# Performance work log

Hardware: AMD Instinct MI355X
Metric: run time of the kernel (lower is better)

Reference implementation:

```python
import jax, jax.numpy as jnp
import numpy as np

B, S, D, V = 32, 1024, 768, 32000


def setup_inputs() -> dict:
    key = jax.random.key(0)
    ks = jax.random.split(key, 12)
    scale = 0.02
    return {
        "tokens": jax.random.randint(ks[0], (B, S), 0, V, dtype=jnp.int32),
        "mask": jax.random.randint(ks[1], (B, S), 0, 2, dtype=jnp.int32),
        "emb": jax.random.normal(ks[2], (V, D), dtype=jnp.float32) * scale,
        "wq": jax.random.normal(ks[3], (D, D), dtype=jnp.float32) * scale,
        "wk": jax.random.normal(ks[4], (D, D), dtype=jnp.float32) * scale,
        "wv": jax.random.normal(ks[5], (D, D), dtype=jnp.float32) * scale,
        "ln_g": jnp.ones((D,), dtype=jnp.float32),
        "ln_b": jnp.zeros((D,), dtype=jnp.float32),
        "w1": jax.random.normal(ks[6], (D, D), dtype=jnp.float32) * scale,
        "b1": jnp.zeros((D,), dtype=jnp.float32),
        "wh": jax.random.normal(ks[7], (D, 2), dtype=jnp.float32) * scale,
        "bh": jnp.zeros((2,), dtype=jnp.float32),
    }


def reference(tokens, mask, emb, wq, wk, wv, ln_g, ln_b, w1, b1, wh, bh):
    # embedding lookup: [B,S,D]
    x = emb[tokens]
    q = x @ wq
    k = x @ wk
    v = x @ wv
    # unscaled attention scores: [B,S,S]
    s = jnp.einsum("bsd,btd->bst", q, k)
    # additive padding mask (mask==1 -> -1e9), broadcast over query dim
    s = s + (-1e9) * mask.astype(s.dtype)[:, None, :]
    a = jax.nn.softmax(s, axis=-1)
    o = jnp.einsum("bst,btd->bsd", a, v)
    # classify on first token
    cls = o[:, 0, :]  # [B,D]
    mu = jnp.mean(cls, axis=-1, keepdims=True)
    var = jnp.var(cls, axis=-1, keepdims=True)
    h = (cls - mu) * jax.lax.rsqrt(var + 1e-5) * ln_g + ln_b
    h = jax.nn.gelu(h @ w1 + b1, approximate=False)
    logits = h @ wh + bh  # [B,2]
    return (logits, a)
```

## Files before the change

kernel.cpp:

```cpp
#include <hip/hip_runtime.h>
#include <hip/hip_bf16.h>

#define NB 32
#define SS 1024
#define DD 768

typedef __attribute__((ext_vector_type(8))) short bf16x8;
typedef __attribute__((ext_vector_type(4))) float f32x4;

__device__ inline ushort f2bf(float f) {
    union { float f; unsigned u; } x;
    x.f = f;
    unsigned r = (x.u + 0x7fffu + ((x.u >> 16) & 1u)) >> 16;
    return (ushort)r;
}

#define GLOBAL_PTR(x) ((const __attribute__((address_space(1))) void*)(x))
#define LDS_PTR(x)    ((__attribute__((address_space(3))) void*)(x))

__global__ void k_cvt(const float* __restrict__ wq, const float* __restrict__ wk,
                      ushort* __restrict__ wqb, ushort* __restrict__ wkb) {
    const int i = (blockIdx.x * 256 + threadIdx.x) * 4;
    const float* src = blockIdx.y ? wk : wq;
    ushort* dst = blockIdx.y ? wkb : wqb;
    const float4 v = *(const float4*)(src + i);
    ushort4 o;
    o.x = f2bf(v.x); o.y = f2bf(v.y); o.z = f2bf(v.z); o.w = f2bf(v.w);
    *(ushort4*)(dst + i) = o;
}

__global__ void k_gather(const int* __restrict__ tokens, const float* __restrict__ emb,
                         ushort* __restrict__ xb) {
    int i = (blockIdx.x * 256 + threadIdx.x) * 4;
    int row = i / DD;
    int col = i - row * DD;
    int tok = tokens[row];
    const float4 v = *(const float4*)(emb + (size_t)tok * DD + col);
    ushort4 o;
    o.x = f2bf(v.x); o.y = f2bf(v.y); o.z = f2bf(v.z); o.w = f2bf(v.w);
    *(ushort4*)(xb + (size_t)row * DD + col) = o;
}

__global__ __launch_bounds__(256, 2) void k_gemm_s(const ushort* __restrict__ A,
                                                   const ushort* __restrict__ Bt,
                                                   ushort* __restrict__ Cb) {
    constexpr int BK = 64;
    __shared__ ushort As[2][128 * BK];
    __shared__ ushort Bs[2][128 * BK];
    const int tid = threadIdx.x;
    const int wave = tid >> 6, lane = tid & 63;
    const int bx = blockIdx.x, by = blockIdx.y;
    const size_t abase = (size_t)bx * 128 * DD;
    const size_t bbase = (size_t)by * 128 * DD;
    const int r = tid >> 3;
    const int cc = (tid & 7) * 8;

    auto stage = [&](int buf, int k0) {
#pragma unroll
        for (int i = 0; i < 4; i++) {
            __builtin_amdgcn_global_load_lds(GLOBAL_PTR(A + abase + (size_t)(r + i * 32) * DD + k0 + cc),
                                             LDS_PTR(&As[buf][(r + i * 32) * BK + cc]), 16, 0, 0);
            __builtin_amdgcn_global_load_lds(GLOBAL_PTR(Bt + bbase + (size_t)(r + i * 32) * DD + k0 + cc),
                                             LDS_PTR(&Bs[buf][(r + i * 32) * BK + cc]), 16, 0, 0);
        }
    };

    f32x4 acc[4][4] = {};
    const int wm = (wave >> 1) * 64, wn = (wave & 1) * 64;
    const int lr = lane & 15, lc = (lane >> 4) * 8;

    stage(0, 0);
    __syncthreads();
    int cur = 0;
#pragma unroll 1
    for (int k0 = 0; k0 < DD; k0 += BK) {
        if (k0 + BK < DD) stage(cur ^ 1, k0 + BK);
        const ushort* as = As[cur];
        const ushort* bs = Bs[cur];
#pragma unroll
        for (int kk = 0; kk < 2; kk++) {
            bf16x8 af[4], bfv[4];
#pragma unroll
            for (int m = 0; m < 4; m++)
                af[m] = *(const bf16x8*)(as + (wm + m * 16 + lr) * BK + kk * 32 + lc);
#pragma unroll
            for (int n = 0; n < 4; n++)
                bfv[n] = *(const bf16x8*)(bs + (wn + n * 16 + lr) * BK + kk * 32 + lc);
#pragma unroll
            for (int m = 0; m < 4; m++)
#pragma unroll
                for (int n = 0; n < 4; n++)
                    acc[m][n] = __builtin_amdgcn_mfma_f32_16x16x32_bf16(af[m], bfv[n], acc[m][n], 0, 0, 0);
        }
        __syncthreads();
        cur ^= 1;
    }
    const int rowbase = bx * 128 + wm + (lane >> 4) * 4;
    const int colbase = by * 128 + wn + (lane & 15);
#pragma unroll
    for (int m = 0; m < 4; m++)
#pragma unroll
        for (int n = 0; n < 4; n++)
#pragma unroll
            for (int j = 0; j < 4; j++)
                Cb[(size_t)(rowbase + m * 16 + j) * DD + colbase + n * 16] = f2bf(acc[m][n][j]);
}

#define HALF_USH (128 * 64)
__global__ __launch_bounds__(512, 2) void k_gemm256(const ushort* __restrict__ A,
                                                    const ushort* __restrict__ Bt,
                                                    ushort* __restrict__ Cb) {
    __shared__ ushort As[2][2][HALF_USH];
    __shared__ ushort Bs[2][2][HALF_USH];
    const int tid = threadIdx.x;
    const int wid = tid >> 6, lane = tid & 63;
    const int wm = wid >> 2, wn = wid & 3;
    const int la = lane & 15;

    const int bx = blockIdx.x, by = blockIdx.y;
    const ushort* Ag = A + (size_t)bx * 256 * DD;
    const ushort* Bg = Bt + (size_t)by * 256 * DD;

    int s_r[2], s_c[2], s_d[2];
#pragma unroll
    for (int l = 0; l < 2; l++) {
        const int L = (l * 512 + tid) * 16;
        const int r = L >> 7;
        const int cb = L & 127;
        s_r[l] = r;
        s_c[l] = (cb ^ ((r & 7) << 4)) >> 1;
        s_d[l] = L >> 1;
    }

    auto stage_half = [&](ushort* dst, const ushort* gsrc) {
#pragma unroll
        for (int l = 0; l < 2; l++)
            __builtin_amdgcn_global_load_lds(GLOBAL_PTR(gsrc + (size_t)s_r[l] * DD + s_c[l]),
                                             LDS_PTR(dst + s_d[l]), 16, 0, 0);
    };

    const int swz = (la & 7) << 4;
    const int off_k0 = (((lane >> 4) << 4) ^ swz) >> 1;
    const int off_k1 = ((64 | ((lane >> 4) << 4)) ^ swz) >> 1;

    f32x4 acc[8][4] = {};

    stage_half(&As[0][0][0], Ag);
    stage_half(&As[0][1][0], Ag + (size_t)128 * DD);
    stage_half(&Bs[0][0][0], Bg);
    stage_half(&Bs[0][1][0], Bg + (size_t)128 * DD);
    __syncthreads();

#pragma unroll 1
    for (int t = 0; t < 12; t++) {
        const int buf = t & 1;
        const ushort* Ah = &As[buf][wm][0];
        const ushort* Bh = &Bs[buf][wn >> 1][0];
        const int brow0 = (wn & 1) * 64;
        const int kt = (t + 1) * 64;
        bf16x8 bfv[4][2];
#pragma unroll
        for (int q = 0; q < 4; q++) {
            if (q == 0) {
#pragma unroll
                for (int n = 0; n < 4; n++) {
                    const int rr = brow0 + n * 16 + la;
                    bfv[n][0] = *(const bf16x8*)(Bh + rr * 64 + off_k0);
                    bfv[n][1] = *(const bf16x8*)(Bh + rr * 64 + off_k1);
                }
            }
            bf16x8 af[2][2];
#pragma unroll
            for (int dm = 0; dm < 2; dm++) {
                const int rr = (q * 2 + dm) * 16 + la;
                af[dm][0] = *(const bf16x8*)(Ah + rr * 64 + off_k0);
                af[dm][1] = *(const bf16x8*)(Ah + rr * 64 + off_k1);
            }
            if (t < 11) {
                if (q == 0) stage_half(&As[buf ^ 1][0][0], Ag + kt);
                if (q == 1) stage_half(&As[buf ^ 1][1][0], Ag + (size_t)128 * DD + kt);
                if (q == 2) stage_half(&Bs[buf ^ 1][0][0], Bg + kt);
                if (q == 3) stage_half(&Bs[buf ^ 1][1][0], Bg + (size_t)128 * DD + kt);
            }
            __builtin_amdgcn_s_setprio(1);
#pragma unroll
            for (int dm = 0; dm < 2; dm++)
#pragma unroll
                for (int n = 0; n < 4; n++)
#pragma unroll
                    for (int kk = 0; kk < 2; kk++)
                        acc[q * 2 + dm][n] = __builtin_amdgcn_mfma_f32_16x16x32_bf16(
                            af[dm][kk], bfv[n][kk], acc[q * 2 + dm][n], 0, 0, 0);
            __builtin_amdgcn_s_setprio(0);
            if (q < 3) __builtin_amdgcn_s_barrier();
        }
        __syncthreads();
    }

    const int rowbase = bx * 256 + wm * 128 + (lane >> 4) * 4;
    const int colbase = by * 256 + wn * 64 + la;
#pragma unroll
    for (int m = 0; m < 8; m++)
#pragma unroll
        for (int n = 0; n < 4; n++)
#pragma unroll
            for (int j = 0; j < 4; j++)
                Cb[(size_t)(rowbase + m * 16 + j) * DD + colbase + n * 16] = f2bf(acc[m][n][j]);
}

__global__ __launch_bounds__(512) void k_attn(const ushort* __restrict__ Y,
                                              const ushort* __restrict__ X,
                                              const int* __restrict__ mask,
                                              float* __restrict__ Aout) {
    __shared__ ushort Ash[2][64 * 64];
    __shared__ int    Msk[SS];
    __shared__ float  RedM[8][64];
    __shared__ float  RedS[8][64];

    const int tid = threadIdx.x;
    const int wid = tid >> 6, lane = tid & 63;
    const int la = lane & 15, lg = lane >> 4;

    const int wgid = blockIdx.x;
    const int g = wgid >> 7, w = wgid & 127;
    const int b = g * 8 + (w & 7);
    const int bx = w >> 3;
    const ushort* Ag = Y + (size_t)b * SS * DD + (size_t)bx * 64 * DD;
    const ushort* Bg = X + (size_t)b * SS * DD;
    float* Ao = Aout + (size_t)b * SS * SS + (size_t)bx * 64 * SS;

    Msk[tid] = mask[b * SS + tid];
    Msk[tid + 512] = mask[b * SS + tid + 512];

    const int r0 = tid >> 3;
    const int cb0 = (tid & 7) << 4;
    const int sc = (cb0 ^ ((r0 & 7) << 4)) >> 1;
    const int dofs = tid * 8;

    const int swz = (la & 7) << 4;
    const int off_k0 = ((lg << 4) ^ swz) >> 1;
    const int off_k1 = ((64 | (lg << 4)) ^ swz) >> 1;

    f32x4 acc[4][8] = {};

    __builtin_amdgcn_global_load_lds(GLOBAL_PTR(Ag + (size_t)r0 * DD + sc),
                                     LDS_PTR(&Ash[0][0] + dofs), 16, 0, 0);
    __syncthreads();

#pragma unroll 1
    for (int t = 0; t < 12; t++) {
        const int k0 = t * 64;
        if (t < 11)
            __builtin_amdgcn_global_load_lds(GLOBAL_PTR(Ag + (size_t)r0 * DD + (k0 + 64) + sc),
                                             LDS_PTR(&Ash[(t + 1) & 1][0] + dofs), 16, 0, 0);
        const ushort* ash = &Ash[t & 1][0];
        bf16x8 af[4][2];
#pragma unroll
        for (int m = 0; m < 4; m++) {
            const int rr = m * 16 + la;
            af[m][0] = *(const bf16x8*)(ash + rr * 64 + off_k0);
            af[m][1] = *(const bf16x8*)(ash + rr * 64 + off_k1);
        }
#pragma unroll
        for (int n = 0; n < 8; n++) {
            const ushort* bp = Bg + (size_t)(wid * 128 + n * 16 + la) * DD + k0 + lg * 8;
            const bf16x8 bf0 = *(const bf16x8*)bp;
            const bf16x8 bf1 = *(const bf16x8*)(bp + 32);
            __builtin_amdgcn_s_setprio(1);
#pragma unroll
            for (int m = 0; m < 4; m++) {
                acc[m][n] = __builtin_amdgcn_mfma_f32_16x16x32_bf16(af[m][0], bf0, acc[m][n], 0, 0, 0);
                acc[m][n] = __builtin_amdgcn_mfma_f32_16x16x32_bf16(af[m][1], bf1, acc[m][n], 0, 0, 0);
            }
            __builtin_amdgcn_s_setprio(0);
        }
        __syncthreads();
    }

    float bias[8];
#pragma unroll
    for (int n = 0; n < 8; n++)
        bias[n] = Msk[wid * 128 + n * 16 + la] ? -1e9f : 0.0f;

    float mxl[4][4];
#pragma unroll
    for (int m = 0; m < 4; m++)
#pragma unroll
        for (int j = 0; j < 4; j++) {
            float v = -3.4e38f;
#pragma unroll
            for (int n = 0; n < 8; n++) v = fmaxf(v, acc[m][n][j] + bias[n]);
#pragma unroll
            for (int off = 1; off < 16; off <<= 1) v = fmaxf(v, __shfl_xor(v, off));
            mxl[m][j] = v;
        }
    if (la == 0) {
#pragma unroll
        for (int m = 0; m < 4; m++)
#pragma unroll
            for (int j = 0; j < 4; j++)
                RedM[wid][m * 16 + lg * 4 + j] = mxl[m][j];
    }
    __syncthreads();
#pragma unroll
    for (int m = 0; m < 4; m++)
#pragma unroll
        for (int j = 0; j < 4; j++) {
            const int r = m * 16 + lg * 4 + j;
            float v = RedM[0][r];
#pragma unroll
            for (int ww = 1; ww < 8; ww++) v = fmaxf(v, RedM[ww][r]);
            mxl[m][j] = v;
        }

    float sml[4][4];
#pragma unroll
    for (int m = 0; m < 4; m++)
#pragma unroll
        for (int j = 0; j < 4; j++) {
            float s = 0.f;
#pragma unroll
            for (int n = 0; n < 8; n++) {
                const float e = __expf(acc[m][n][j] + bias[n] - mxl[m][j]);
                acc[m][n][j] = e;
                s += e;
            }
#pragma unroll
            for (int off = 1; off < 16; off <<= 1) s += __shfl_xor(s, off);
            sml[m][j] = s;
        }
    if (la == 0) {
#pragma unroll
        for (int m = 0; m < 4; m++)
#pragma unroll
            for (int j = 0; j < 4; j++)
                RedS[wid][m * 16 + lg * 4 + j] = sml[m][j];
    }
    __syncthreads();
#pragma unroll
    for (int m = 0; m < 4; m++)
#pragma unroll
        for (int j = 0; j < 4; j++) {
            const int r = m * 16 + lg * 4 + j;
            float s = RedS[0][r];
#pragma unroll
            for (int ww = 1; ww < 8; ww++) s += RedS[ww][r];
            const float inv = 1.0f / s;
#pragma unroll
            for (int n = 0; n < 8; n++)
                Ao[(size_t)r * SS + wid * 128 + n * 16 + la] = acc[m][n][j] * inv;
        }
}

__global__ __launch_bounds__(256) void k_xbar(const float* __restrict__ a, const int* __restrict__ tokens,
                                              const float* __restrict__ emb, float* __restrict__ part) {
    const int b = blockIdx.x >> 3, c = blockIdx.x & 7;
    __shared__ float a0s[128];
    __shared__ int toks[128];
    const int tid = threadIdx.x;
    if (tid < 128) {
        a0s[tid] = a[(size_t)b * SS * SS + c * 128 + tid];
        toks[tid] = tokens[b * SS + c * 128 + tid];
    }
    __syncthreads();
    float acc0 = 0.f, acc1 = 0.f, acc2 = 0.f;
#pragma unroll 4
    for (int t = 0; t < 128; t++) {
        const float at = a0s[t];
        const float* er = emb + (size_t)toks[t] * DD;
        acc0 = fmaf(at, er[tid], acc0);
        acc1 = fmaf(at, er[tid + 256], acc1);
        acc2 = fmaf(at, er[tid + 512], acc2);
    }
    float* p = part + ((size_t)c * NB + b) * DD;
    p[tid] = acc0; p[tid + 256] = acc1; p[tid + 512] = acc2;
}

__global__ __launch_bounds__(128) void k_cls(const float* __restrict__ part, const float* __restrict__ wv,
                                             float* __restrict__ cls) {
    const int b = blockIdx.y, tid = threadIdx.x;
    const int c = blockIdx.x * 128 + tid;
    __shared__ float xb[DD];
#pragma unroll
    for (int j = 0; j < 6; j++) {
        const int k = tid + j * 128;
        float s = 0.f;
#pragma unroll
        for (int p = 0; p < 8; p++) s += part[((size_t)p * NB + b) * DD + k];
        xb[k] = s;
    }
    __syncthreads();
    float acc = 0.f;
#pragma unroll 8
    for (int k = 0; k < DD; k++) acc = fmaf(xb[k], wv[(size_t)k * DD + c], acc);
    cls[(size_t)b * DD + c] = acc;
}

__device__ inline float block_sum256(float v, float* red, int tid) {
#pragma unroll
    for (int off = 32; off; off >>= 1) v += __shfl_xor(v, off);
    __syncthreads();
    if ((tid & 63) == 0) red[tid >> 6] = v;
    __syncthreads();
    return red[0] + red[1] + red[2] + red[3];
}

__global__ __launch_bounds__(256) void k_ln(const float* __restrict__ cls, const float* __restrict__ ln_g,
                                            const float* __restrict__ ln_b, float* __restrict__ hs) {
    const int b = blockIdx.x, tid = threadIdx.x;
    __shared__ float red[4];
    float v[3];
#pragma unroll
    for (int j = 0; j < 3; j++) v[j] = cls[(size_t)b * DD + tid + j * 256];
    const float mu = block_sum256(v[0] + v[1] + v[2], red, tid) * (1.0f / DD);
    float dv = 0.f;
#pragma unroll
    for (int j = 0; j < 3; j++) { const float d = v[j] - mu; dv += d * d; }
    __syncthreads();
    const float var = block_sum256(dv, red, tid) * (1.0f / DD);
    const float sc = 1.0f / sqrtf(var + 1e-5f);
#pragma unroll
    for (int j = 0; j < 3; j++) {
        const int d = tid + j * 256;
        hs[(size_t)b * DD + d] = (v[j] - mu) * sc * ln_g[d] + ln_b[d];
    }
}

__global__ __launch_bounds__(128) void k_mlp(const float* __restrict__ hs, const float* __restrict__ w1,
                                             const float* __restrict__ b1, const float* __restrict__ wh,
                                             float* __restrict__ part_l) {
    const int b = blockIdx.y, tid = threadIdx.x;
    const int j = blockIdx.x * 128 + tid;
    __shared__ float h[DD];
#pragma unroll
    for (int q = 0; q < 6; q++) h[tid + q * 128] = hs[(size_t)b * DD + tid + q * 128];
    __syncthreads();
    float p = b1[j];
#pragma unroll 8
    for (int d = 0; d < DD; d++) p = fmaf(h[d], w1[(size_t)d * DD + j], p);
    const float g = 0.5f * p * (1.0f + erff(p * 0.70710678118654752f));
    float l0 = g * wh[j * 2 + 0];
    float l1 = g * wh[j * 2 + 1];
#pragma unroll
    for (int off = 32; off; off >>= 1) { l0 += __shfl_xor(l0, off); l1 += __shfl_xor(l1, off); }
    __shared__ float r0[2], r1[2];
    if ((tid & 63) == 0) { r0[tid >> 6] = l0; r1[tid >> 6] = l1; }
    __syncthreads();
    if (tid == 0) {
        part_l[((size_t)b * 6 + blockIdx.x) * 2 + 0] = r0[0] + r0[1];
        part_l[((size_t)b * 6 + blockIdx.x) * 2 + 1] = r1[0] + r1[1];
    }
}

__global__ __launch_bounds__(64) void k_final(const float* __restrict__ part_l, const float* __restrict__ bh,
                                              float* __restrict__ out) {
    const int b = threadIdx.x;
    if (b < NB) {
        float l0 = bh[0], l1 = bh[1];
#pragma unroll
        for (int c = 0; c < 6; c++) {
            l0 += part_l[((size_t)b * 6 + c) * 2 + 0];
            l1 += part_l[((size_t)b * 6 + c) * 2 + 1];
        }
        out[b * 2 + 0] = l0;
        out[b * 2 + 1] = l1;
    }
}

extern "C" void kernel_launch(void* const* d_in, const int* in_sizes, int n_in,
                              void* d_out, int out_size, void* d_ws, size_t ws_size,
                              hipStream_t stream) {
    const int*   tokens = (const int*)d_in[0];
    const int*   mask   = (const int*)d_in[1];
    const float* emb    = (const float*)d_in[2];
    const float* wq     = (const float*)d_in[3];
    const float* wk     = (const float*)d_in[4];
    const float* wv     = (const float*)d_in[5];
    const float* ln_g   = (const float*)d_in[6];
    const float* ln_b   = (const float*)d_in[7];
    const float* w1     = (const float*)d_in[8];
    const float* b1     = (const float*)d_in[9];
    const float* wh     = (const float*)d_in[10];
    const float* bh     = (const float*)d_in[11];
    float* out = (float*)d_out;

    char* ws = (char*)d_ws;
    const size_t XB = (size_t)NB * SS * DD * 2;
    const size_t WB = (size_t)DD * DD * 2;
    ushort* xb  = (ushort*)ws;
    ushort* yb  = (ushort*)(ws + XB);
    ushort* wqb = (ushort*)(ws + 2 * XB);
    ushort* wkb = (ushort*)(ws + 2 * XB + WB);
    ushort* Wt  = (ushort*)(ws + 2 * XB + 2 * WB);
    char*   p4  = ws + 2 * XB + 3 * WB;
    float*  part   = (float*)p4;
    float*  cls    = (float*)(p4 + 786432);
    float*  hsb    = (float*)(p4 + 786432 + 98304);
    float*  part_l = (float*)(p4 + 786432 + 2 * 98304);

    float* a_region = out + 64;

    k_cvt<<<dim3(576, 2), 256, 0, stream>>>(wq, wk, wqb, wkb);
    k_gather<<<24576, 256, 0, stream>>>(tokens, emb, xb);
    k_gemm_s<<<dim3(6, 6), 256, 0, stream>>>(wkb, wqb, Wt);
    k_gemm256<<<dim3(128, 3), 512, 0, stream>>>(xb, Wt, yb);
    k_attn<<<512, 512, 0, stream>>>(yb, xb, mask, a_region);
    k_xbar<<<256, 256, 0, stream>>>(a_region, tokens, emb, part);
    k_cls<<<dim3(6, NB), 128, 0, stream>>>(part, wv, cls);
    k_ln<<<NB, 256, 0, stream>>>(cls, ln_g, ln_b, hsb);
    k_mlp<<<dim3(6, NB), 128, 0, stream>>>(hsb, w1, b1, wh, part_l);
    k_final<<<1, 64, 0, stream>>>(part_l, bh, out);
}
```

Before: 346.1 us.

## Stage attention K operand through LDS and drop specialized 256-tile GEMM

The attention-score kernel now stages the full 1024-row key operand into double-buffered LDS in 32-wide K slices with an XOR swizzle, instead of having each wave read its B fragments straight from global memory. The K loop doubles to 24 steps of single MFMA pairs. Separately, the dedicated 256x256 projection GEMM is removed and the generic 128-tile GEMM kernel is used for the Y = X·Wt product. This trades higher LDS usage (about 136KB, which limits occupancy to one block) and more barriers for fewer uncoalesced global loads. Dropping the tuned large-tile GEMM may cost throughput.

```diff
diff --git a/kernel.cpp b/kernel.cpp
--- a/kernel.cpp
+++ b/kernel.cpp
@@ -106,113 +106,12 @@
                 Cb[(size_t)(rowbase + m * 16 + j) * DD + colbase + n * 16] = f2bf(acc[m][n][j]);
 }
 
-#define HALF_USH (128 * 64)
-__global__ __launch_bounds__(512, 2) void k_gemm256(const ushort* __restrict__ A,
-                                                    const ushort* __restrict__ Bt,
-                                                    ushort* __restrict__ Cb) {
-    __shared__ ushort As[2][2][HALF_USH];
-    __shared__ ushort Bs[2][2][HALF_USH];
-    const int tid = threadIdx.x;
-    const int wid = tid >> 6, lane = tid & 63;
-    const int wm = wid >> 2, wn = wid & 3;
-    const int la = lane & 15;
-
-    const int bx = blockIdx.x, by = blockIdx.y;
-    const ushort* Ag = A + (size_t)bx * 256 * DD;
-    const ushort* Bg = Bt + (size_t)by * 256 * DD;
-
-    int s_r[2], s_c[2], s_d[2];
-#pragma unroll
-    for (int l = 0; l < 2; l++) {
-        const int L = (l * 512 + tid) * 16;
-        const int r = L >> 7;
-        const int cb = L & 127;
-        s_r[l] = r;
-        s_c[l] = (cb ^ ((r & 7) << 4)) >> 1;
-        s_d[l] = L >> 1;
-    }
-
-    auto stage_half = [&](ushort* dst, const ushort* gsrc) {
-#pragma unroll
-        for (int l = 0; l < 2; l++)
-            __builtin_amdgcn_global_load_lds(GLOBAL_PTR(gsrc + (size_t)s_r[l] * DD + s_c[l]),
-                                             LDS_PTR(dst + s_d[l]), 16, 0, 0);
-    };
-
-    const int swz = (la & 7) << 4;
-    const int off_k0 = (((lane >> 4) << 4) ^ swz) >> 1;
-    const int off_k1 = ((64 | ((lane >> 4) << 4)) ^ swz) >> 1;
-
-    f32x4 acc[8][4] = {};
-
-    stage_half(&As[0][0][0], Ag);
-    stage_half(&As[0][1][0], Ag + (size_t)128 * DD);
-    stage_half(&Bs[0][0][0], Bg);
-    stage_half(&Bs[0][1][0], Bg + (size_t)128 * DD);
-    __syncthreads();
-
-#pragma unroll 1
-    for (int t = 0; t < 12; t++) {
-        const int buf = t & 1;
-        const ushort* Ah = &As[buf][wm][0];
-        const ushort* Bh = &Bs[buf][wn >> 1][0];
-        const int brow0 = (wn & 1) * 64;
-        const int kt = (t + 1) * 64;
-        bf16x8 bfv[4][2];
-#pragma unroll
-        for (int q = 0; q < 4; q++) {
-            if (q == 0) {
-#pragma unroll
-                for (int n = 0; n < 4; n++) {
-                    const int rr = brow0 + n * 16 + la;
-                    bfv[n][0] = *(const bf16x8*)(Bh + rr * 64 + off_k0);
-                    bfv[n][1] = *(const bf16x8*)(Bh + rr * 64 + off_k1);
-                }
-            }
-            bf16x8 af[2][2];
-#pragma unroll
-            for (int dm = 0; dm < 2; dm++) {
-                const int rr = (q * 2 + dm) * 16 + la;
-                af[dm][0] = *(const bf16x8*)(Ah + rr * 64 + off_k0);
-                af[dm][1] = *(const bf16x8*)(Ah + rr * 64 + off_k1);
-            }
-            if (t < 11) {
-                if (q == 0) stage_half(&As[buf ^ 1][0][0], Ag + kt);
-                if (q == 1) stage_half(&As[buf ^ 1][1][0], Ag + (size_t)128 * DD + kt);
-                if (q == 2) stage_half(&Bs[buf ^ 1][0][0], Bg + kt);
-                if (q == 3) stage_half(&Bs[buf ^ 1][1][0], Bg + (size_t)128 * DD + kt);
-            }
-            __builtin_amdgcn_s_setprio(1);
-#pragma unroll
-            for (int dm = 0; dm < 2; dm++)
-#pragma unroll
-                for (int n = 0; n < 4; n++)
-#pragma unroll
-                    for (int kk = 0; kk < 2; kk++)
-                        acc[q * 2 + dm][n] = __builtin_amdgcn_mfma_f32_16x16x32_bf16(
-                            af[dm][kk], bfv[n][kk], acc[q * 2 + dm][n], 0, 0, 0);
-            __builtin_amdgcn_s_setprio(0);
-            if (q < 3) __builtin_amdgcn_s_barrier();
-        }
-        __syncthreads();
-    }
-
-    const int rowbase = bx * 256 + wm * 128 + (lane >> 4) * 4;
-    const int colbase = by * 256 + wn * 64 + la;
-#pragma unroll
-    for (int m = 0; m < 8; m++)
-#pragma unroll
-        for (int n = 0; n < 4; n++)
-#pragma unroll
-            for (int j = 0; j < 4; j++)
-                Cb[(size_t)(rowbase + m * 16 + j) * DD + colbase + n * 16] = f2bf(acc[m][n][j]);
-}
-
 __global__ __launch_bounds__(512) void k_attn(const ushort* __restrict__ Y,
                                               const ushort* __restrict__ X,
                                               const int* __restrict__ mask,
                                               float* __restrict__ Aout) {
-    __shared__ ushort Ash[2][64 * 64];
+    __shared__ ushort Bsh[2][SS * 32];
+    __shared__ ushort Ash[2][64 * 32];
     __shared__ int    Msk[SS];
     __shared__ float  RedM[8][64];
     __shared__ float  RedS[8][64];
@@ -232,46 +131,54 @@
     Msk[tid] = mask[b * SS + tid];
     Msk[tid + 512] = mask[b * SS + tid + 512];
 
-    const int r0 = tid >> 3;
-    const int cb0 = (tid & 7) << 4;
-    const int sc = (cb0 ^ ((r0 & 7) << 4)) >> 1;
-    const int dofs = tid * 8;
-
-    const int swz = (la & 7) << 4;
-    const int off_k0 = ((lg << 4) ^ swz) >> 1;
-    const int off_k1 = ((64 | (lg << 4)) ^ swz) >> 1;
+    auto stageB = [&](ushort* dst, const ushort* gsrc) {
+#pragma unroll
+        for (int l = 0; l < 8; l++) {
+            const int L = (l * 512 + tid) * 16;
+            const int r = L >> 6;
+            const int scol = ((L & 63) ^ ((r & 3) << 4)) >> 1;
+            __builtin_amdgcn_global_load_lds(GLOBAL_PTR(gsrc + (size_t)r * DD + scol),
+                                             LDS_PTR(dst + (L >> 1)), 16, 0, 0);
+        }
+    };
+    auto stageA = [&](ushort* dst, const ushort* gsrc) {
+        if (tid < 256) {
+            const int L = tid * 16;
+            const int r = L >> 6;
+            const int scol = ((L & 63) ^ ((r & 3) << 4)) >> 1;
+            __builtin_amdgcn_global_load_lds(GLOBAL_PTR(gsrc + (size_t)r * DD + scol),
+                                             LDS_PTR(dst + (L >> 1)), 16, 0, 0);
+        }
+    };
+
+    const int koff = ((lg ^ (la & 3)) << 3);
 
     f32x4 acc[4][8] = {};
 
-    __builtin_amdgcn_global_load_lds(GLOBAL_PTR(Ag + (size_t)r0 * DD + sc),
-                                     LDS_PTR(&Ash[0][0] + dofs), 16, 0, 0);
+    stageA(&Ash[0][0], Ag);
+    stageB(&Bsh[0][0], Bg);
     __syncthreads();
 
 #pragma unroll 1
-    for (int t = 0; t < 12; t++) {
-        const int k0 = t * 64;
-        if (t < 11)
-            __builtin_amdgcn_global_load_lds(GLOBAL_PTR(Ag + (size_t)r0 * DD + (k0 + 64) + sc),
-                                             LDS_PTR(&Ash[(t + 1) & 1][0] + dofs), 16, 0, 0);
+    for (int t = 0; t < 24; t++) {
+        if (t < 23) {
+            const int k1 = (t + 1) * 32;
+            stageA(&Ash[(t + 1) & 1][0], Ag + k1);
+            stageB(&Bsh[(t + 1) & 1][0], Bg + k1);
+        }
         const ushort* ash = &Ash[t & 1][0];
-        bf16x8 af[4][2];
-#pragma unroll
-        for (int m = 0; m < 4; m++) {
-            const int rr = m * 16 + la;
-            af[m][0] = *(const bf16x8*)(ash + rr * 64 + off_k0);
-            af[m][1] = *(const bf16x8*)(ash + rr * 64 + off_k1);
-        }
+        const ushort* bsh = &Bsh[t & 1][0];
+        bf16x8 af[4];
+#pragma unroll
+        for (int m = 0; m < 4; m++)
+            af[m] = *(const bf16x8*)(ash + (m * 16 + la) * 32 + koff);
 #pragma unroll
         for (int n = 0; n < 8; n++) {
-            const ushort* bp = Bg + (size_t)(wid * 128 + n * 16 + la) * DD + k0 + lg * 8;
-            const bf16x8 bf0 = *(const bf16x8*)bp;
-            const bf16x8 bf1 = *(const bf16x8*)(bp + 32);
+            const bf16x8 bf = *(const bf16x8*)(bsh + (wid * 128 + n * 16 + la) * 32 + koff);
             __builtin_amdgcn_s_setprio(1);
 #pragma unroll
-            for (int m = 0; m < 4; m++) {
-                acc[m][n] = __builtin_amdgcn_mfma_f32_16x16x32_bf16(af[m][0], bf0, acc[m][n], 0, 0, 0);
-                acc[m][n] = __builtin_amdgcn_mfma_f32_16x16x32_bf16(af[m][1], bf1, acc[m][n], 0, 0, 0);
-            }
+            for (int m = 0; m < 4; m++)
+                acc[m][n] = __builtin_amdgcn_mfma_f32_16x16x32_bf16(af[m], bf, acc[m][n], 0, 0, 0);
             __builtin_amdgcn_s_setprio(0);
         }
         __syncthreads();
@@ -503,7 +410,7 @@
     k_cvt<<<dim3(576, 2), 256, 0, stream>>>(wq, wk, wqb, wkb);
     k_gather<<<24576, 256, 0, stream>>>(tokens, emb, xb);
     k_gemm_s<<<dim3(6, 6), 256, 0, stream>>>(wkb, wqb, Wt);
-    k_gemm256<<<dim3(128, 3), 512, 0, stream>>>(xb, Wt, yb);
+    k_gemm_s<<<dim3(256, 6), 256, 0, stream>>>(xb, Wt, yb);
     k_attn<<<512, 512, 0, stream>>>(yb, xb, mask, a_region);
     k_xbar<<<256, 256, 0, stream>>>(a_region, tokens, emb, part);
     k_cls<<<dim3(6, NB), 128, 0, stream>>>(part, wv, cls);
```

Result: no change. 348.8 us (+0.8%).
